# Kernel tuning notes

Measured on AMD Instinct MI355X. Metric: run time of the kernel, lower is better.

## Reference

```python
import jax, jax.numpy as jnp
import numpy as np

NEG_SLOPE = 0.2


def gat_layer(x, src, dst, W, a_src, a_dst, b, concat):
    # x: [N, F_in], W: [F_in, H*C], a_src/a_dst: [H, C], b: [H*C] or [C]
    N = x.shape[0]
    H, C = a_src.shape
    h = (x @ W).reshape(N, H, C)                       # per-head projections
    al_s = jnp.einsum('nhc,hc->nh', h, a_src)          # [N, H]
    al_d = jnp.einsum('nhc,hc->nh', h, a_dst)          # [N, H]
    e = jax.nn.leaky_relu(al_s[src] + al_d[dst], NEG_SLOPE)  # [E, H]
    # softmax over incoming edges of each destination node
    m = jax.ops.segment_max(e, dst, num_segments=N)    # [N, H]
    ex = jnp.exp(e - m[dst])
    s = jax.ops.segment_sum(ex, dst, num_segments=N)   # [N, H]
    alpha = ex / (s[dst] + 1e-16)                      # [E, H]
    msg = h[src] * alpha[:, :, None]                   # [E, H, C]
    out = jax.ops.segment_sum(msg, dst, num_segments=N)  # [N, H, C]
    out = out.reshape(N, H * C) if concat else out.mean(axis=1)
    return out + b


def setup_inputs() -> dict:
    key = jax.random.key(0)
    ks = jax.random.split(key, 12)
    N, E, F_in, HID, H, NCLS = 100000, 1600000, 128, 32, 4, 40
    x = jax.random.normal(ks[0], (N, F_in), dtype=jnp.float32)
    edge_index = jax.random.randint(ks[1], (2, E), 0, N, dtype=jnp.int32)
    W1 = jax.random.normal(ks[2], (F_in, H * HID), dtype=jnp.float32) * 0.1
    as1 = jax.random.normal(ks[3], (H, HID), dtype=jnp.float32) * 0.1
    ad1 = jax.random.normal(ks[4], (H, HID), dtype=jnp.float32) * 0.1
    b1 = jnp.zeros((H * HID,), dtype=jnp.float32)
    W2 = jax.random.normal(ks[5], (H * HID, H * NCLS), dtype=jnp.float32) * 0.1
    as2 = jax.random.normal(ks[6], (H, NCLS), dtype=jnp.float32) * 0.1
    ad2 = jax.random.normal(ks[7], (H, NCLS), dtype=jnp.float32) * 0.1
    b2 = jnp.zeros((NCLS,), dtype=jnp.float32)
    return {"x": x, "edge_index": edge_index, "W1": W1, "as1": as1,
            "ad1": ad1, "b1": b1, "W2": W2, "as2": as2, "ad2": ad2, "b2": b2}


def reference(x, edge_index, W1, as1, ad1, b1, W2, as2, ad2, b2):
    src, dst = edge_index[0], edge_index[1]
    h = gat_layer(x, src, dst, W1, as1, ad1, b1, concat=True)
    h = jax.nn.relu(h)  # dropout=0.0 -> identity
    out = gat_layer(h, src, dst, W2, as2, ad2, b2, concat=False)
    return jax.nn.log_softmax(out, axis=-1)
```

## Files before the change

kernel.cpp:

```cpp
#include <hip/hip_runtime.h>

typedef short short8 __attribute__((ext_vector_type(8)));
typedef float f32x4 __attribute__((ext_vector_type(4)));
typedef int   i32x4 __attribute__((ext_vector_type(4)));
typedef unsigned short u16;
typedef unsigned int u32;

__device__ __forceinline__ float b2f(u16 u){ union{u32 i; float f;} v; v.i=((u32)u)<<16; return v.f; }
__device__ __forceinline__ u16 f2b(float f){ union{float f; u32 i;} v; v.f=f; return (u16)((v.i + 0x7fffu + ((v.i>>16)&1u))>>16); }
__device__ __forceinline__ float loadv(const void* p, long i, bool isbf){
  return isbf ? b2f(((const u16*)p)[i]) : ((const float*)p)[i];
}

__global__ void detect_bf16(const void* x, int n, int* flag){
  __shared__ int cnt;
  if (threadIdx.x==0) cnt = 0;
  __syncthreads();
  int m = n < 4096 ? n : 4096;
  int good = 0;
  for (int i = threadIdx.x; i < m; i += 256){
    u16 u = ((const u16*)x)[i];
    int e = (u >> 7) & 0xff;
    if (u == 0 || (e >= 100 && e <= 140)) good++;
  }
  atomicAdd(&cnt, good);
  __syncthreads();
  if (threadIdx.x==0){
    flag[0] = (cnt >= (m*3)/4) ? 1 : 0;
    flag[1] = 1;
  }
}

__global__ __launch_bounds__(256) void convw(const void* __restrict__ W, u16* __restrict__ WT,
                                             int M, const int* __restrict__ flag){
  const bool wbf = *flag != 0;
  int i = blockIdx.x*256 + threadIdx.x;
  if (i >= 128*M) return;
  int k = i / M, c = i - k*M;
  WT[c*128 + k] = wbf ? ((const u16*)W)[i] : f2b(((const float*)W)[i]);
}

__global__ __launch_bounds__(256) void count_1p(const int* __restrict__ dst, int* __restrict__ counts, int E){
  int i = blockIdx.x*256 + threadIdx.x;
  int stride = gridDim.x*256;
  for (int e = i; e < E; e += stride) atomicAdd(&counts[dst[e]], 1);
}

__global__ __launch_bounds__(256) void scatter_1p(const int* __restrict__ src, const int* __restrict__ dst,
    const int* __restrict__ rp, int* __restrict__ cur, int* __restrict__ psrc, int E){
  int i = blockIdx.x*256 + threadIdx.x;
  int stride = gridDim.x*256;
  for (int e = i; e < E; e += stride){
    int d = dst[e];
    int pos = rp[d] + atomicAdd(&cur[d], 1);
    psrc[pos] = src[e];
  }
}

__global__ __launch_bounds__(256) void scan_bsum(const int* __restrict__ counts, int* __restrict__ bsum, int N){
  __shared__ int sm[256];
  int t = threadIdx.x, i = blockIdx.x*256 + t;
  sm[t] = (i < N) ? counts[i] : 0;
  __syncthreads();
  for (int off = 128; off; off >>= 1){
    if (t < off) sm[t] += sm[t+off];
    __syncthreads();
  }
  if (t == 0) bsum[blockIdx.x] = sm[0];
}

__global__ __launch_bounds__(1024) void scan_top(const int* __restrict__ bsum, int* __restrict__ bscan, int B){
  __shared__ int sm[1024];
  int t = threadIdx.x;
  int v = (t < B) ? bsum[t] : 0;
  sm[t] = v;
  __syncthreads();
  for (int off = 1; off < 1024; off <<= 1){
    int x = (t >= off) ? sm[t-off] : 0;
    __syncthreads();
    sm[t] += x;
    __syncthreads();
  }
  if (t < B) bscan[t] = sm[t] - v;
}

__global__ __launch_bounds__(256) void scan_final(const int* __restrict__ counts, const int* __restrict__ bscan,
                                                  int* __restrict__ rp, int N, int E){
  __shared__ int sm[256];
  int t = threadIdx.x, i = blockIdx.x*256 + t;
  int v = (i < N) ? counts[i] : 0;
  sm[t] = v;
  __syncthreads();
  for (int off = 1; off < 256; off <<= 1){
    int x = (t >= off) ? sm[t-off] : 0;
    __syncthreads();
    sm[t] += x;
    __syncthreads();
  }
  if (i < N) rp[i] = bscan[blockIdx.x] + sm[t] - v;
  if (i == 0) rp[N] = E;
}

template<int M>
__global__ __launch_bounds__(256) void gemm_k(const void* __restrict__ X, const u16* __restrict__ WT,
                                              u16* __restrict__ OUT, u16* __restrict__ OUT2, int N,
                                              const int* __restrict__ flagX){
  __shared__ u16 wt[M][136];
  const bool xbf = *flagX != 0;
  int tid = threadIdx.x;
  for (int i = tid; i < M*16; i += 256){
    int c = i >> 4, k8 = (i & 15) << 3;
    *(short8*)&wt[c][k8] = *(const short8*)&WT[c*128 + k8];
  }
  __syncthreads();
  int wave = tid >> 6, lane = tid & 63;
  int quad = lane >> 4, l16 = lane & 15;
  int rowbase = blockIdx.x*64 + wave*16;
  int rr = rowbase + l16; if (rr >= N) rr = N-1;
  const int NT = M/16;
  f32x4 acc[NT];
  #pragma unroll
  for (int t=0;t<NT;t++) acc[t] = (f32x4){0.f,0.f,0.f,0.f};
  #pragma unroll
  for (int kt = 0; kt < 4; kt++){
    int kb = kt*32 + quad*8;
    short8 a;
    if (xbf){
      a = *(const short8*)((const u16*)X + (size_t)rr*128 + kb);
    } else {
      const float* xf = (const float*)X + (size_t)rr*128 + kb;
      #pragma unroll
      for (int j=0;j<8;j++) a[j] = (short)f2b(xf[j]);
    }
    #pragma unroll
    for (int t=0;t<NT;t++){
      short8 b = *(const short8*)&wt[t*16 + l16][kb];
      acc[t] = __builtin_amdgcn_mfma_f32_16x16x32_bf16(a, b, acc[t], 0, 0, 0);
    }
  }
  #pragma unroll
  for (int t=0;t<NT;t++){
    #pragma unroll
    for (int r=0;r<4;r++){
      int row = rowbase + quad*4 + r;
      if (row < N){
        u16 val = f2b(acc[t][r]);
        if (M > 128 && t*16 >= 128) OUT2[(size_t)row*32 + (t*16 - 128) + l16] = val;
        else                        OUT [(size_t)row*128 + t*16 + l16]        = val;
      }
    }
  }
}

template<int C>
__global__ __launch_bounds__(256) void al_k(const u16* __restrict__ Hm, const void* __restrict__ as_,
                     const void* __restrict__ ad_,
                     float* __restrict__ als, float* __restrict__ ald, int N, const int* __restrict__ flag){
  __shared__ float s_as[4*C], s_ad[4*C];
  const bool isbf = *flag != 0;
  for (int i = threadIdx.x; i < 4*C; i += 256){
    s_as[i] = loadv(as_, i, isbf);
    s_ad[i] = loadv(ad_, i, isbf);
  }
  __syncthreads();
  int idx = blockIdx.x*256 + threadIdx.x;
  if (idx >= N*4) return;
  int n = idx >> 2, h = idx & 3;
  const short8* row = (const short8*)(Hm + (size_t)n*(4*C) + h*C);
  float ss = 0.f, sd = 0.f;
  #pragma unroll
  for (int v = 0; v < C/8; v++){
    short8 pk = row[v];
    #pragma unroll
    for (int j = 0; j < 8; j++){
      union{u32 i; float f;} u; u.i = ((u32)(u16)pk[j]) << 16;
      ss += u.f * s_as[h*C + v*8 + j];
      sd += u.f * s_ad[h*C + v*8 + j];
    }
  }
  als[idx] = ss;
  ald[idx] = sd;
}

__global__ __launch_bounds__(256) void al2_k(const u16* __restrict__ Hm, const u16* __restrict__ Ht,
                     const void* __restrict__ as_, const void* __restrict__ ad_,
                     float* __restrict__ als, float* __restrict__ ald, int N, const int* __restrict__ flag){
  __shared__ float s_as[160], s_ad[160];
  const bool isbf = *flag != 0;
  for (int i = threadIdx.x; i < 160; i += 256){
    s_as[i] = loadv(as_, i, isbf);
    s_ad[i] = loadv(ad_, i, isbf);
  }
  __syncthreads();
  int idx = blockIdx.x*256 + threadIdx.x;
  if (idx >= N*4) return;
  int n = idx >> 2, h = idx & 3;
  float ss = 0.f, sd = 0.f;
  int c0 = h*40;
  #pragma unroll
  for (int v = 0; v < 5; v++){
    int c = c0 + v*8;
    const u16* p = (c < 128) ? (Hm + (size_t)n*128 + c) : (Ht + (size_t)n*32 + (c - 128));
    short8 pk = *(const short8*)p;
    #pragma unroll
    for (int j = 0; j < 8; j++){
      union{u32 i; float f;} u; u.i = ((u32)(u16)pk[j]) << 16;
      ss += u.f * s_as[c + j];
      sd += u.f * s_ad[c + j];
    }
  }
  als[idx] = ss;
  ald[idx] = sd;
}

__global__ __launch_bounds__(256) void agg1(const u16* __restrict__ h1,
    const float* __restrict__ als, const float* __restrict__ ald, const void* __restrict__ b1,
    const int* __restrict__ rp, const int* __restrict__ psrc,
    u16* __restrict__ hrelu, int N, const int* __restrict__ flag){
  __shared__ __align__(16) int   sbuf[4][16];
  __shared__ __align__(16) float ebT[4][4*20];
  const bool isbf = *flag != 0;
  int wave = threadIdx.x >> 6, lane = threadIdx.x & 63;
  int node = blockIdx.x*4 + wave;
  bool live = node < N;
  int nd = live ? node : 0;
  int hd = lane >> 4;
  int eidx = lane >> 2, hA = lane & 3;
  int beg = __builtin_amdgcn_readfirstlane(rp[nd]);
  int end = __builtin_amdgcn_readfirstlane(rp[nd+1]);
  if (!live){ beg = 0; end = 0; }
  float advA = ald[nd*4 + hA];
  const char* hb = (const char*)h1;
  int lane4 = lane << 2;
  int* sb = sbuf[wave];
  float* eb = ebT[wave];
  float a0 = 0.f, a1 = 0.f;
  float sp = 0.f;
  for (int cbeg = beg; cbeg < end; cbeg += 16){
    int cnt = min(16, end - cbeg);
    int e = cbeg + eidx;
    bool vv = e < end;
    int ec = vv ? e : beg;
    int s = psrc[ec];
    float lv = als[s*4 + hA] + advA;
    lv = fmaxf(lv, 0.2f*lv);
    float ex = vv ? __expf(lv) : 0.f;
    sp += ex;
    eb[hA*20 + eidx] = ex;
    if (hA == 0) sb[eidx] = vv ? (s << 8) : 0;
    for (int j0 = 0; j0 < cnt; j0 += 4){
      i32x4 off4 = *(const i32x4*)&sb[j0];
      f32x4 ex4  = *(const f32x4*)&eb[hd*20 + j0];
      u32 p[4];
      #pragma unroll
      for (int i=0;i<4;i++) p[i] = *(const u32*)(hb + (u32)(off4[i] + lane4));
      #pragma unroll
      for (int i=0;i<4;i++){
        union{u32 u; float f;} w;
        w.u = p[i] << 16;         a0 += ex4[i]*w.f;
        w.u = p[i] & 0xffff0000u; a1 += ex4[i]*w.f;
      }
    }
  }
  sp += __shfl_xor(sp, 4);  sp += __shfl_xor(sp, 8);
  sp += __shfl_xor(sp, 16); sp += __shfl_xor(sp, 32);
  float sum = __shfl(sp, hd);
  if (live){
    float inv = 1.f/(sum + 1e-16f);
    float v0 = a0*inv + loadv(b1, 2*lane,     isbf);
    float v1 = a1*inv + loadv(b1, 2*lane + 1, isbf);
    v0 = v0 > 0.f ? v0 : 0.f;
    v1 = v1 > 0.f ? v1 : 0.f;
    u32 packed = (u32)f2b(v0) | ((u32)f2b(v1) << 16);
    *(u32*)(hrelu + (size_t)node*128 + 2*lane) = packed;
  }
}

__global__ __launch_bounds__(256) void agg2(const u16* __restrict__ h2m, const u16* __restrict__ h2t,
    const float* __restrict__ als, const float* __restrict__ ald, const void* __restrict__ b2,
    const int* __restrict__ rp, const int* __restrict__ psrc,
    void* __restrict__ out, int N, const int* __restrict__ flag){
  __shared__ __align__(16) int   sbuf[4][16];
  __shared__ __align__(16) float ebT[4][4*20];
  __shared__ __align__(16) float sm[4][160];
  const bool isbf = *flag != 0;
  int wave = threadIdx.x >> 6, lane = threadIdx.x & 63;
  int node = blockIdx.x*4 + wave;
  bool live = node < N;
  int nd = live ? node : 0;
  int g = lane >> 4, s = lane & 15;
  int hm = s / 5;
  int moff = s << 4;
  int tof  = s << 2;
  int eidx = lane >> 2, hA = lane & 3;
  int beg = __builtin_amdgcn_readfirstlane(rp[nd]);
  int end = __builtin_amdgcn_readfirstlane(rp[nd+1]);
  if (!live){ beg = 0; end = 0; }
  float advA = ald[nd*4 + hA];
  const char* hbm = (const char*)h2m;
  const char* hbt = (const char*)h2t;
  int* sb = sbuf[wave];
  float* eb = ebT[wave];
  float am[8] = {0.f,0.f,0.f,0.f,0.f,0.f,0.f,0.f};
  float at0 = 0.f, at1 = 0.f;
  float sp = 0.f;
  for (int cbeg = beg; cbeg < end; cbeg += 16){
    int cnt = min(16, end - cbeg);
    int e = cbeg + eidx;
    bool vv = e < end;
    int ec = vv ? e : beg;
    int src = psrc[ec];
    float lv = als[src*4 + hA] + advA;
    lv = fmaxf(lv, 0.2f*lv);
    float ex = vv ? __expf(lv) : 0.f;
    sp += ex;
    eb[hA*20 + eidx] = ex;
    if (hA == 0) sb[eidx] = vv ? src : 0;
    for (int j0 = 0; j0 < cnt; j0 += 4){
      int sv    = sb[j0 + g];
      float exm = eb[hm*20 + j0 + g];
      float ext = eb[3*20  + j0 + g];
      i32x4 P = *(const i32x4*)(hbm + ((((u32)sv) << 8) + moff));
      u32   q = *(const u32*) (hbt + ((((u32)sv) << 6) + tof));
      union{u32 u; float f;} w;
      #pragma unroll
      for (int i=0;i<4;i++){
        u32 pv = (u32)P[i];
        w.u = pv << 16;         am[2*i]   += exm*w.f;
        w.u = pv & 0xffff0000u; am[2*i+1] += exm*w.f;
      }
      w.u = q << 16;         at0 += ext*w.f;
      w.u = q & 0xffff0000u; at1 += ext*w.f;
    }
  }
  sp += __shfl_xor(sp, 4);  sp += __shfl_xor(sp, 8);
  sp += __shfl_xor(sp, 16); sp += __shfl_xor(sp, 32);
  float Sm = __shfl(sp, hm);
  float S3 = __shfl(sp, 3);
  #pragma unroll
  for (int k=0;k<8;k++){ am[k] += __shfl_xor(am[k],16); am[k] += __shfl_xor(am[k],32); }
  at0 += __shfl_xor(at0,16); at0 += __shfl_xor(at0,32);
  at1 += __shfl_xor(at1,16); at1 += __shfl_xor(at1,32);
  if (lane < 16){
    float invm = 1.f/(Sm + 1e-16f);
    float invt = 1.f/(S3 + 1e-16f);
    f32x4 v0 = {am[0]*invm, am[1]*invm, am[2]*invm, am[3]*invm};
    f32x4 v1 = {am[4]*invm, am[5]*invm, am[6]*invm, am[7]*invm};
    *(f32x4*)&sm[wave][8*s]     = v0;
    *(f32x4*)&sm[wave][8*s + 4] = v1;
    sm[wave][128 + 2*s] = at0*invt;
    sm[wave][129 + 2*s] = at1*invt;
  }
  __syncthreads();
  float v = -__builtin_inff();
  if (lane < 40)
    v = (sm[wave][lane] + sm[wave][40+lane] + sm[wave][80+lane] + sm[wave][120+lane]) * 0.25f
        + loadv(b2, lane, isbf);
  float mxo = v;
  for (int o = 32; o; o >>= 1) mxo = fmaxf(mxo, __shfl_xor(mxo, o));
  float exl = (lane < 40) ? __expf(v - mxo) : 0.f;
  float S = exl;
  for (int o = 32; o; o >>= 1) S += __shfl_xor(S, o);
  if (live && lane < 40){
    float r = v - mxo - __logf(S);
    if (isbf) ((u16*)out)[(size_t)node*40 + lane] = f2b(r);
    else      ((float*)out)[(size_t)node*40 + lane] = r;
  }
}

extern "C" void kernel_launch(void* const* d_in, const int* in_sizes, int n_in,
                              void* d_out, int out_size, void* d_ws, size_t ws_size,
                              hipStream_t stream){
  const void* x   = d_in[0];
  const int*  ei  = (const int*)d_in[1];
  const void* W1  = d_in[2];
  const void* as1 = d_in[3];
  const void* ad1 = d_in[4];
  const void* b1  = d_in[5];
  const void* W2  = d_in[6];
  const void* as2 = d_in[7];
  const void* ad2 = d_in[8];
  const void* b2  = d_in[9];

  const int N = in_sizes[0] / 128;
  const int E = in_sizes[1] / 2;
  const int* esrc = ei;
  const int* edst = ei + E;

  char* w = (char*)d_ws;
  size_t off = 0;
  auto take = [&](size_t bytes)->void*{
    void* p = w + off;
    off = (off + bytes + 255) & ~(size_t)255;
    return p;
  };
  u16*   h12    = (u16*)take((size_t)N*128*2);
  u16*   h2t    = (u16*)take((size_t)N*32*2);
  u16*   hrelu  = (u16*)take((size_t)N*128*2);
  float* als1   = (float*)take((size_t)N*4*4);
  float* ald1   = (float*)take((size_t)N*4*4);
  float* als2   = (float*)take((size_t)N*4*4);
  float* ald2   = (float*)take((size_t)N*4*4);
  int*   rowptr = (int*)take((size_t)(N+1)*4);
  int*   counts = (int*)take((size_t)N*4);
  int*   bsum   = (int*)take(1024*4);
  int*   bscan  = (int*)take(1024*4);
  int*   psrc   = (int*)take((size_t)E*4);
  int*   flag   = (int*)take(64);
  u16*   wt1    = (u16*)take(128*128*2);
  u16*   wt2    = (u16*)take(160*128*2);

  const int B = (N + 255) / 256;

  detect_bf16<<<1, 256, 0, stream>>>(x, N*128, flag);
  convw<<<(128*128+255)/256, 256, 0, stream>>>(W1, wt1, 128, flag);
  convw<<<(128*160+255)/256, 256, 0, stream>>>(W2, wt2, 160, flag);

  hipMemsetAsync(counts, 0, (size_t)N*4, stream);
  count_1p<<<2048, 256, 0, stream>>>(edst, counts, E);
  scan_bsum<<<B, 256, 0, stream>>>(counts, bsum, N);
  scan_top<<<1, 1024, 0, stream>>>(bsum, bscan, B);
  scan_final<<<B, 256, 0, stream>>>(counts, bscan, rowptr, N, E);
  hipMemsetAsync(counts, 0, (size_t)N*4, stream);
  scatter_1p<<<2048, 256, 0, stream>>>(esrc, edst, rowptr, counts, psrc, E);

  gemm_k<128><<<(N+63)/64, 256, 0, stream>>>(x, wt1, h12, h2t , N, flag);
  al_k<32><<<(4*N+255)/256, 256, 0, stream>>>(h12, as1, ad1, als1, ald1, N, flag);
  agg1<<<(N+3)/4, 256, 0, stream>>>(h12, als1, ald1, b1, rowptr, psrc, hrelu, N, flag);

  gemm_k<160><<<(N+63)/64, 256, 0, stream>>>(hrelu, wt2, h12, h2t, N, flag+1);
  al2_k<<<(4*N+255)/256, 256, 0, stream>>>(h12, h2t, as2, ad2, als2, ald2, N, flag);
  agg2<<<(N+3)/4, 256, 0, stream>>>(h12, h2t, als2, ald2, b2, rowptr, psrc, d_out, N, flag);
}
```

Measured before the change: 526.7 us.

## Partition CSR count and scatter by destination range per XCD

Replaces the grid-stride edge count and scatter kernels with versions where each block handles one edge chunk and only the destination nodes in one of eight ranges, selected by blockIdx & 7. The intent is that blocks dispatched round-robin to the same XCD touch a disjoint slice of the counts, cursor and psrc arrays, keeping atomics local to one L2 and cutting cross-die coherence traffic. In exchange every edge's dst (and src for matching edges) is read eight times, which multiplies global read traffic.

```diff
diff --git a/kernel.cpp b/kernel.cpp
--- a/kernel.cpp
+++ b/kernel.cpp
@@ -40,20 +40,35 @@
   WT[c*128 + k] = wbf ? ((const u16*)W)[i] : f2b(((const float*)W)[i]);
 }
 
-__global__ __launch_bounds__(256) void count_1p(const int* __restrict__ dst, int* __restrict__ counts, int E){
-  int i = blockIdx.x*256 + threadIdx.x;
-  int stride = gridDim.x*256;
-  for (int e = i; e < E; e += stride) atomicAdd(&counts[dst[e]], 1);
-}
-
-__global__ __launch_bounds__(256) void scatter_1p(const int* __restrict__ src, const int* __restrict__ dst,
-    const int* __restrict__ rp, int* __restrict__ cur, int* __restrict__ psrc, int E){
-  int i = blockIdx.x*256 + threadIdx.x;
-  int stride = gridDim.x*256;
-  for (int e = i; e < E; e += stride){
+__global__ __launch_bounds__(256) void count_x(const int* __restrict__ dst,
+    int* __restrict__ counts, int E, int N, int nchunk){
+  int r = blockIdx.x & 7;
+  int chunk = blockIdx.x >> 3;
+  int lo = (int)(((long)N * r) >> 3);
+  int hi = (int)(((long)N * (r+1)) >> 3);
+  int per = (E + nchunk - 1) / nchunk;
+  int s = chunk * per, t = min(E, s + per);
+  for (int e = s + threadIdx.x; e < t; e += 256){
     int d = dst[e];
-    int pos = rp[d] + atomicAdd(&cur[d], 1);
-    psrc[pos] = src[e];
+    if (d >= lo && d < hi) atomicAdd(&counts[d], 1);
+  }
+}
+
+__global__ __launch_bounds__(256) void scatter_x(const int* __restrict__ src, const int* __restrict__ dst,
+    const int* __restrict__ rp, int* __restrict__ cur,
+    int* __restrict__ psrc, int E, int N, int nchunk){
+  int r = blockIdx.x & 7;
+  int chunk = blockIdx.x >> 3;
+  int lo = (int)(((long)N * r) >> 3);
+  int hi = (int)(((long)N * (r+1)) >> 3);
+  int per = (E + nchunk - 1) / nchunk;
+  int s = chunk * per, t = min(E, s + per);
+  for (int e = s + threadIdx.x; e < t; e += 256){
+    int d = dst[e];
+    if (d >= lo && d < hi){
+      int pos = rp[d] + atomicAdd(&cur[d], 1);
+      psrc[pos] = src[e];
+    }
   }
 }
 
@@ -411,18 +426,19 @@
   u16*   wt2    = (u16*)take(160*128*2);
 
   const int B = (N + 255) / 256;
+  const int NCHUNK = 128;
 
   detect_bf16<<<1, 256, 0, stream>>>(x, N*128, flag);
   convw<<<(128*128+255)/256, 256, 0, stream>>>(W1, wt1, 128, flag);
   convw<<<(128*160+255)/256, 256, 0, stream>>>(W2, wt2, 160, flag);
 
   hipMemsetAsync(counts, 0, (size_t)N*4, stream);
-  count_1p<<<2048, 256, 0, stream>>>(edst, counts, E);
+  count_x<<<8*NCHUNK, 256, 0, stream>>>(edst, counts, E, N, NCHUNK);
   scan_bsum<<<B, 256, 0, stream>>>(counts, bsum, N);
   scan_top<<<1, 1024, 0, stream>>>(bsum, bscan, B);
   scan_final<<<B, 256, 0, stream>>>(counts, bscan, rowptr, N, E);
   hipMemsetAsync(counts, 0, (size_t)N*4, stream);
-  scatter_1p<<<2048, 256, 0, stream>>>(esrc, edst, rowptr, counts, psrc, E);
+  scatter_x<<<8*NCHUNK, 256, 0, stream>>>(esrc, edst, rowptr, counts, psrc, E, N, NCHUNK);
 
   gemm_k<128><<<(N+63)/64, 256, 0, stream>>>(x, wt1, h12, h2t , N, flag);
   al_k<32><<<(4*N+255)/256, 256, 0, stream>>>(h12, as1, ad1, als1, ald1, N, flag);
```

Measured after the change: 486.5 us. 1.08x faster.
